# Performance work log

Hardware: AMD Instinct MI355X
Metric: run time of the kernel (lower is better)

The kernel has to match this reference:

```python
import jax, jax.numpy as jnp
import numpy as np

DIM, DEPTH, HEADS, DIM_HEAD, MLP = 1024, 4, 16, 64, 4096
INNER = HEADS * DIM_HEAD
B, N = 2, 1024


def _ln(x, g, b, eps=1e-5):
    mu = jnp.mean(x, axis=-1, keepdims=True)
    var = jnp.mean(jnp.square(x - mu), axis=-1, keepdims=True)
    return (x - mu) * jax.lax.rsqrt(var + eps) * g + b


def setup_inputs() -> dict:
    key = jax.random.key(0)
    ks = jax.random.split(key, 8)
    s = 0.02
    return {
        "x": jax.random.normal(ks[0], (B, N, DIM), jnp.float32),
        "mask": jax.random.randint(ks[1], (B, N, N), 0, 2, jnp.int32),
        "ln1_g": jnp.ones((DEPTH, DIM), jnp.float32),
        "ln1_b": jnp.zeros((DEPTH, DIM), jnp.float32),
        "qkv_w": jax.random.normal(ks[2], (DEPTH, DIM, 3 * INNER), jnp.float32) * s,
        "out_w": jax.random.normal(ks[3], (DEPTH, INNER, DIM), jnp.float32) * s,
        "out_b": jnp.zeros((DEPTH, DIM), jnp.float32),
        "ln2_g": jnp.ones((DEPTH, DIM), jnp.float32),
        "ln2_b": jnp.zeros((DEPTH, DIM), jnp.float32),
        "ff1_w": jax.random.normal(ks[4], (DEPTH, DIM, MLP), jnp.float32) * s,
        "ff1_b": jnp.zeros((DEPTH, MLP), jnp.float32),
        "ff2_w": jax.random.normal(ks[5], (DEPTH, MLP, DIM), jnp.float32) * s,
        "ff2_b": jnp.zeros((DEPTH, DIM), jnp.float32),
    }


def reference(x, mask, ln1_g, ln1_b, qkv_w, out_w, out_b, ln2_g, ln2_b,
              ff1_w, ff1_b, ff2_w, ff2_b):
    scale = DIM_HEAD ** -0.5
    masked = (mask == 0)[:, None, :, :]  # [B,1,N,N], True -> fill -1e9
    b, n, _ = x.shape
    for l in range(DEPTH):
        # --- prenorm attention ---
        h = _ln(x, ln1_g[l], ln1_b[l])
        qkv = h @ qkv_w[l]  # [B,N,3*INNER]
        q, k, v = jnp.split(qkv, 3, axis=-1)
        q = q.reshape(b, n, HEADS, DIM_HEAD).transpose(0, 2, 1, 3)
        k = k.reshape(b, n, HEADS, DIM_HEAD).transpose(0, 2, 1, 3)
        v = v.reshape(b, n, HEADS, DIM_HEAD).transpose(0, 2, 1, 3)
        dots = jnp.einsum('bhqd,bhkd->bhqk', q, k) * scale
        dots = jnp.where(masked, jnp.float32(-1e9), dots)
        attn = jax.nn.softmax(dots, axis=-1)
        o = jnp.einsum('bhqk,bhkd->bhqd', attn, v)
        o = o.transpose(0, 2, 1, 3).reshape(b, n, INNER)
        x = o @ out_w[l] + out_b[l] + x
        # --- prenorm feedforward ---
        h = _ln(x, ln2_g[l], ln2_b[l])
        h = jax.nn.gelu(h @ ff1_w[l] + ff1_b[l], approximate=False)
        x = h @ ff2_w[l] + ff2_b[l] + x
    return x
```

## Files before the change

kernel.cpp:

```cpp
#include <hip/hip_runtime.h>
#include <stdint.h>

#define DIMM 1024
#define NSEQ 1024
#define BB 2
#define HEADSN 16
#define MLPD 4096
#define DEPTHN 4
#define MROWS (BB*NSEQ)
#define VSTR 10240

typedef __bf16 bf16x8 __attribute__((ext_vector_type(8)));
typedef float f32x4 __attribute__((ext_vector_type(4)));

__device__ __forceinline__ float bf2f(unsigned short u) {
    union { uint32_t i; float f; } x; x.i = ((uint32_t)u) << 16; return x.f;
}
__device__ __forceinline__ unsigned short f2bf(float f) {
    union { uint32_t i; float f; } x; x.f = f;
    uint32_t r = x.i + 0x7fffu + ((x.i >> 16) & 1u);
    return (unsigned short)(r >> 16);
}
__device__ __forceinline__ float loadf(const void* p, size_t i, int f32) {
    return f32 ? ((const float*)p)[i] : bf2f(((const unsigned short*)p)[i]);
}
__device__ __forceinline__ uint32_t cvt_pk_bf16(float lo, float hi) {
    uint32_t r;
    asm("v_cvt_pk_bf16_f32 %0, %1, %2" : "=v"(r) : "v"(lo), "v"(hi));
    return r;
}

__device__ __forceinline__ void gl_lds16(const unsigned short* g, unsigned short* l) {
    __builtin_amdgcn_global_load_lds(
        (const __attribute__((address_space(1))) uint32_t*)g,
        (__attribute__((address_space(3))) uint32_t*)l,
        16, 0, 0);
}

__device__ __forceinline__ void wait_vm4() { asm volatile("s_waitcnt vmcnt(4)" ::: "memory"); }
__device__ __forceinline__ void wait_vm0() { asm volatile("s_waitcnt vmcnt(0)" ::: "memory"); }
__device__ __forceinline__ void barrier_sync() {
    asm volatile("" ::: "memory");
    __builtin_amdgcn_s_barrier();
    asm volatile("" ::: "memory");
}

__global__ __launch_bounds__(256) void sniff_kernel(const unsigned short* __restrict__ x,
                                                    int* __restrict__ flag) {
    __shared__ int cnt[256];
    int tid = threadIdx.x;
    int c = 0;
    for (int i = tid * 2; i < 65536; i += 512) {
        int e = (x[i] >> 7) & 0xFF;
        if (e >= 0x8A) c++;
    }
    cnt[tid] = c;
    __syncthreads();
    for (int s = 128; s > 0; s >>= 1) {
        if (tid < s) cnt[tid] += cnt[tid + s];
        __syncthreads();
    }
    if (tid == 0) flag[0] = (cnt[0] > 32) ? 1 : 0;
}

__global__ __launch_bounds__(256) void store_out(const float* __restrict__ xf, void* __restrict__ out,
                                                 const int* __restrict__ flag) {
    int f = flag[0];
    int i = blockIdx.x * 256 + threadIdx.x;
    float v = xf[i];
    if (f) ((float*)out)[i] = v;
    else   ((unsigned short*)out)[i] = f2bf(v);
}
__global__ __launch_bounds__(256) void conv_all(const void* s0, const void* s1, const void* s2,
                                                const void* s3, const void* s4, const void* s5,
                                                const void* s6, unsigned short* __restrict__ dst,
                                                const int* __restrict__ flag) {
    int f = flag[0];
    const void* src; int len, off;
    switch (blockIdx.y) {
        case 0: src = s0; len = 1024; off = 0;    break;
        case 1: src = s1; len = 1024; off = 1024; break;
        case 2: src = s2; len = 1024; off = 2048; break;
        case 3: src = s3; len = 1024; off = 3072; break;
        case 4: src = s4; len = 1024; off = 4096; break;
        case 5: src = s5; len = 1024; off = 5120; break;
        default: src = s6; len = 4096; off = 6144; break;
    }
    int i = blockIdx.x * 256 + threadIdx.x;
    if (i < DEPTHN * len) {
        int l = i / len, o = i - l * len;
        dst[l * VSTR + off + o] = f2bf(loadf(src, i, f));
    }
}

__global__ __launch_bounds__(256) void transpose_conv(const void* __restrict__ in, size_t srcOffE,
                                                      unsigned short* __restrict__ out,
                                                      int K, int N, const int* __restrict__ flag) {
    int f = flag[0];
    __shared__ unsigned short t[32][33];
    int n0 = blockIdx.x * 32, k0 = blockIdx.y * 32;
    int tx = threadIdx.x, ty = threadIdx.y;
#pragma unroll
    for (int i = 0; i < 4; i++) {
        int k = k0 + ty + i * 8;
        t[ty + i * 8][tx] = f2bf(loadf(in, srcOffE + (size_t)k * N + n0 + tx, f));
    }
    __syncthreads();
#pragma unroll
    for (int i = 0; i < 4; i++) {
        int n = n0 + ty + i * 8;
        out[(size_t)n * K + k0 + tx] = t[tx][ty + i * 8];
    }
}

__global__ __launch_bounds__(256) void transpose_attn(const void* __restrict__ qkvw,
                                                      const void* __restrict__ outw,
                                                      int layer, unsigned short* __restrict__ wT,
                                                      const int* __restrict__ flag) {
    int f = flag[0];
    __shared__ unsigned short t[32][33];
    int id = blockIdx.x;
    const void* src; int N; size_t soff; unsigned short* dst; int bx, by;
    if (id < 3072) {
        N = 3072; bx = id % 96; by = id / 96;
        src = qkvw; soff = (size_t)layer * 1024 * 3072; dst = wT;
    } else {
        id -= 3072; N = 1024; bx = id % 32; by = id / 32;
        src = outw; soff = (size_t)layer * 1024 * 1024; dst = wT + 3 * 1024 * 1024;
    }
    int n0 = bx * 32, k0 = by * 32;
    int tx = threadIdx.x, ty = threadIdx.y;
#pragma unroll
    for (int i = 0; i < 4; i++) {
        int k = k0 + ty + i * 8;
        t[ty + i * 8][tx] = f2bf(loadf(src, soff + (size_t)k * N + n0 + tx, f));
    }
    __syncthreads();
#pragma unroll
    for (int i = 0; i < 4; i++) {
        int n = n0 + ty + i * 8;
        dst[(size_t)n * 1024 + k0 + tx] = t[tx][ty + i * 8];
    }
}

__global__ __launch_bounds__(256) void vt_kernel(const unsigned short* __restrict__ qkv,
                                                 unsigned short* __restrict__ vt) {
    __shared__ unsigned short t[32][33];
    int b = blockIdx.z;
    int c0 = blockIdx.x * 32, k0 = blockIdx.y * 32;
    int tx = threadIdx.x, ty = threadIdx.y;
#pragma unroll
    for (int i = 0; i < 4; i++) {
        int k = k0 + ty + i * 8;
        t[ty + i * 8][tx] = qkv[(size_t)(b * 1024 + k) * 3072 + 2048 + c0 + tx];
    }
    __syncthreads();
#pragma unroll
    for (int i = 0; i < 4; i++) {
        int c = c0 + ty + i * 8;
        vt[(size_t)(b * 1024 + c) * 1024 + k0 + tx] = t[tx][ty + i * 8];
    }
}

__global__ __launch_bounds__(256) void mask_pack(const int* __restrict__ mask,
                                                 unsigned long long* __restrict__ bits) {
    int wid = (blockIdx.x * 256 + threadIdx.x) >> 6;
    int lane = threadIdx.x & 63;
#pragma unroll
    for (int i = 0; i < 16; i++) {
        int w = wid * 16 + i;
        int mv = mask[(size_t)w * 64 + lane];
        unsigned long long bl = __ballot(mv != 0);
        if (lane == 0) bits[w] = bl;
    }
}

__global__ __launch_bounds__(256) void ln_raw(const void* __restrict__ x, float* __restrict__ xf,
                                              const unsigned short* __restrict__ g,
                                              const unsigned short* __restrict__ bta,
                                              unsigned short* __restrict__ out,
                                              const int* __restrict__ flag) {
    int f = flag[0];
    int row = blockIdx.x, tid = threadIdx.x;
    size_t base = (size_t)row * DIMM;
    float v[4]; float s = 0.f, s2 = 0.f;
#pragma unroll
    for (int i = 0; i < 4; i++) {
        int c = tid + i * 256;
        v[i] = loadf(x, base + c, f);
        xf[base + c] = v[i];
        s += v[i]; s2 += v[i] * v[i];
    }
#pragma unroll
    for (int off = 32; off >= 1; off >>= 1) {
        s  += __shfl_down(s, off, 64);
        s2 += __shfl_down(s2, off, 64);
    }
    __shared__ float rs[4], rs2[4];
    int wv = tid >> 6;
    if ((tid & 63) == 0) { rs[wv] = s; rs2[wv] = s2; }
    __syncthreads();
    s  = rs[0] + rs[1] + rs[2] + rs[3];
    s2 = rs2[0] + rs2[1] + rs2[2] + rs2[3];
    float mu  = s * (1.f / DIMM);
    float var = s2 * (1.f / DIMM) - mu * mu;
    float rr  = rsqrtf(var + 1e-5f);
#pragma unroll
    for (int i = 0; i < 4; i++) {
        int c = tid + i * 256;
        float y = (v[i] - mu) * rr * bf2f(g[c]) + bf2f(bta[c]);
        out[base + c] = f2bf(y);
    }
}

__global__ __launch_bounds__(256) void ln_kernel(const float* __restrict__ x,
                                                 const unsigned short* __restrict__ g,
                                                 const unsigned short* __restrict__ bta,
                                                 unsigned short* __restrict__ out) {
    int row = blockIdx.x, tid = threadIdx.x;
    const float* xr = x + (size_t)row * DIMM;
    float v[4]; float s = 0.f, s2 = 0.f;
#pragma unroll
    for (int i = 0; i < 4; i++) { v[i] = xr[tid + i * 256]; s += v[i]; s2 += v[i] * v[i]; }
#pragma unroll
    for (int off = 32; off >= 1; off >>= 1) {
        s  += __shfl_down(s, off, 64);
        s2 += __shfl_down(s2, off, 64);
    }
    __shared__ float rs[4], rs2[4];
    int wv = tid >> 6;
    if ((tid & 63) == 0) { rs[wv] = s; rs2[wv] = s2; }
    __syncthreads();
    s  = rs[0] + rs[1] + rs[2] + rs[3];
    s2 = rs2[0] + rs2[1] + rs2[2] + rs2[3];
    float mu  = s * (1.f / DIMM);
    float var = s2 * (1.f / DIMM) - mu * mu;
    float rr  = rsqrtf(var + 1e-5f);
#pragma unroll
    for (int i = 0; i < 4; i++) {
        int c = tid + i * 256;
        float y = (v[i] - mu) * rr * bf2f(g[c]) + bf2f(bta[c]);
        out[(size_t)row * DIMM + c] = f2bf(y);
    }
}

template <int S, int HAS_LN>
__global__ __launch_bounds__(256) void reduce_ln(const float* __restrict__ slab,
                                                 const unsigned short* __restrict__ bias,
                                                 float* __restrict__ xf,
                                                 const unsigned short* __restrict__ g,
                                                 const unsigned short* __restrict__ bta,
                                                 unsigned short* __restrict__ out) {
    const size_t SL = (size_t)MROWS * DIMM;
    int row = blockIdx.x, tid = threadIdx.x;
    float v[4]; float s = 0.f, s2 = 0.f;
#pragma unroll
    for (int i = 0; i < 4; i++) {
        int c = tid + i * 256;
        size_t idx = (size_t)row * DIMM + c;
        float t = xf[idx] + bf2f(bias[c]);
#pragma unroll
        for (int z = 0; z < S; z++) t += slab[z * SL + idx];
        xf[idx] = t;
        v[i] = t; s += t; s2 += t * t;
    }
    if (HAS_LN) {
#pragma unroll
        for (int off = 32; off >= 1; off >>= 1) {
            s  += __shfl_down(s, off, 64);
            s2 += __shfl_down(s2, off, 64);
        }
        __shared__ float rs[4], rs2[4];
        int wv = tid >> 6;
        if ((tid & 63) == 0) { rs[wv] = s; rs2[wv] = s2; }
        __syncthreads();
        s  = rs[0] + rs[1] + rs[2] + rs[3];
        s2 = rs2[0] + rs2[1] + rs2[2] + rs2[3];
        float mu  = s * (1.f / DIMM);
        float var = s2 * (1.f / DIMM) - mu * mu;
        float rr  = rsqrtf(var + 1e-5f);
#pragma unroll
        for (int i = 0; i < 4; i++) {
            int c = tid + i * 256;
            float y = (v[i] - mu) * rr * bf2f(g[c]) + bf2f(bta[c]);
            out[(size_t)row * DIMM + c] = f2bf(y);
        }
    }
}

template <int MODE, int SPLITK>
__global__ __launch_bounds__(512) void gemm_bt(const unsigned short* __restrict__ A,
                                               const unsigned short* __restrict__ Bt,
                                               const unsigned short* __restrict__ bias,
                                               unsigned short* __restrict__ Cbf,
                                               float* __restrict__ Cres,
                                               int M, int N, int K) {
    __shared__ __align__(16) unsigned short As0[128 * 64];
    __shared__ __align__(16) unsigned short Bs0[128 * 64];
    __shared__ __align__(16) unsigned short As1[128 * 64];
    __shared__ __align__(16) unsigned short Bs1[128 * 64];
    const int tid = threadIdx.x;
    const int mBase = blockIdx.y * 128, nBase = blockIdx.x * 128;
    const int w = tid >> 6, lane = tid & 63;
    const int wm = (w >> 2) * 64, wn = (w & 3) * 32;
    const int quad = lane >> 4, l16 = lane & 15;
    const int kLen = K / SPLITK;
    const int kStart = (SPLITK > 1) ? blockIdx.z * kLen : 0;
    const int NT = kLen / 64;

    f32x4 acc[4][2];
#pragma unroll
    for (int i = 0; i < 4; i++)
#pragma unroll
        for (int j = 0; j < 2; j++) acc[i][j] = (f32x4){0.f, 0.f, 0.f, 0.f};

    const int wb = w & 3;
    const int lr8 = lane >> 3;
    const int sgran = (lane & 7) ^ lr8;
    const unsigned short* G = (w < 4 ? A  + (size_t)(mBase + wb * 32 + lr8) * K
                                     : Bt + (size_t)(nBase + wb * 32 + lr8) * K)
                              + kStart + sgran * 8;
    unsigned short* S0 = (w < 4 ? As0 : Bs0) + (wb * 32) * 64;
    unsigned short* S1 = (w < 4 ? As1 : Bs1) + (wb * 32) * 64;
    const size_t r8 = (size_t)8 * K;

    const int rg0 = (quad ^ (l16 & 7)) * 8;
    const int rg1 = ((4 + quad) ^ (l16 & 7)) * 8;

    auto stage = [&](unsigned short* S, int t) {
        const unsigned short* g = G + (size_t)t * 64;
#pragma unroll
        for (int i = 0; i < 4; i++)
            gl_lds16(g + (size_t)i * r8, S + i * 8 * 64);
    };
    auto compute = [&](const unsigned short* Asb, const unsigned short* Bsb) {
#pragma unroll
        for (int ks = 0; ks < 2; ks++) {
            const int rg = ks ? rg1 : rg0;
            bf16x8 af[4], bfv[2];
#pragma unroll
            for (int i = 0; i < 4; i++)
                af[i] = *(const bf16x8*)&Asb[(wm + i * 16 + l16) * 64 + rg];
#pragma unroll
            for (int j = 0; j < 2; j++)
                bfv[j] = *(const bf16x8*)&Bsb[(wn + j * 16 + l16) * 64 + rg];
#pragma unroll
            for (int i = 0; i < 4; i++)
#pragma unroll
                for (int j = 0; j < 2; j++)
                    acc[i][j] = __builtin_amdgcn_mfma_f32_16x16x32_bf16(af[i], bfv[j], acc[i][j], 0, 0, 0);
        }
    };

    stage(S0, 0);
    for (int t = 0; t < NT; t += 2) {
        stage(S1, t + 1);
        wait_vm4();
        barrier_sync();
        compute(As0, Bs0);
        barrier_sync();
        if (t + 2 < NT) {
            stage(S0, t + 2);
            wait_vm4();
        } else {
            wait_vm0();
        }
        barrier_sync();
        compute(As1, Bs1);
        barrier_sync();
    }

    const size_t slabOff = (MODE == 3) ? (size_t)blockIdx.z * M * N : 0;
#pragma unroll
    for (int i = 0; i < 4; i++) {
#pragma unroll
        for (int j = 0; j < 2; j++) {
#pragma unroll
            for (int r = 0; r < 4; r++) {
                int m = mBase + wm + i * 16 + quad * 4 + r;
                int n = nBase + wn + j * 16 + l16;
                float v = acc[i][j][r];
                size_t idx = (size_t)m * N + n;
                if (MODE == 0) {
                    Cbf[idx] = f2bf(v);
                } else if (MODE == 1) {
                    if (SPLITK > 1) {
                        if (blockIdx.z == 0) v += bf2f(bias[n]);
                        atomicAdd(&Cres[idx], v);
                    } else {
                        Cres[idx] += v + bf2f(bias[n]);
                    }
                } else if (MODE == 2) {
                    float t2 = v + bf2f(bias[n]);
                    float gg = 0.5f * t2 * (1.f + erff(t2 * 0.70710678118f));
                    Cbf[idx] = f2bf(gg);
                } else {
                    Cres[slabOff + idx] = v;
                }
            }
        }
    }
}

__global__ __launch_bounds__(256) void attn_mfma(const unsigned short* __restrict__ qkv,
                                                 const unsigned short* __restrict__ vt,
                                                 const unsigned long long* __restrict__ mbits,
                                                 unsigned short* __restrict__ o) {
    __shared__ __align__(16) unsigned short Ks[64 * 72];
    __shared__ __align__(16) unsigned short Vs[64 * 72];

    const int tid = threadIdx.x, w = tid >> 6, lane = tid & 63;
    const int quad = lane >> 4, l16 = lane & 15;
    const int qt = blockIdx.x, h = blockIdx.y, b = blockIdx.z;

    const size_t qrow = (size_t)(b * NSEQ + qt * 64 + w * 16 + l16) * 3072 + h * 64;
    bf16x8 qf[2];
    qf[0] = *(const bf16x8*)(qkv + qrow + quad * 8);
    qf[1] = *(const bf16x8*)(qkv + qrow + 32 + quad * 8);

    const int srow = tid >> 2, scol = (tid & 3) * 16;
    const unsigned short* kg_base = qkv + (size_t)(b * NSEQ) * 3072 + 1024 + h * 64;
    const unsigned short* vg_base = vt + (size_t)((b * HEADSN + h) * 64 + srow) * 1024;

    f32x4 oacc[4];
#pragma unroll
    for (int j = 0; j < 4; j++) oacc[j] = (f32x4){0.f, 0.f, 0.f, 0.f};
    float m_run = -1e30f, l_run = 0.f;

    const unsigned long long* mb = mbits + ((size_t)(b * NSEQ + qt * 64 + w * 16 + l16)) * 16;

    for (int kt = 0; kt < 16; kt++) {
        __syncthreads();
        {
            const unsigned short* kg = kg_base + (size_t)(kt * 64 + srow) * 3072 + scol;
            uint4 k0 = *(const uint4*)kg;
            uint4 k1 = *(const uint4*)(kg + 8);
            const unsigned short* vg = vg_base + kt * 64 + scol;
            uint4 v0 = *(const uint4*)vg;
            uint4 v1 = *(const uint4*)(vg + 8);
            *(uint4*)&Ks[srow * 72 + scol]     = k0;
            *(uint4*)&Ks[srow * 72 + scol + 8] = k1;
            *(uint4*)&Vs[srow * 72 + scol]     = v0;
            *(uint4*)&Vs[srow * 72 + scol + 8] = v1;
        }
        __syncthreads();

        f32x4 sacc[4];
#pragma unroll
        for (int j = 0; j < 4; j++) sacc[j] = (f32x4){0.f, 0.f, 0.f, 0.f};
#pragma unroll
        for (int ks = 0; ks < 2; ks++) {
#pragma unroll
            for (int j = 0; j < 4; j++) {
                bf16x8 kf = *(const bf16x8*)&Ks[(j * 16 + l16) * 72 + ks * 32 + quad * 8];
                sacc[j] = __builtin_amdgcn_mfma_f32_16x16x32_bf16(kf, qf[ks], sacc[j], 0, 0, 0);
            }
        }

        const unsigned long long mw = mb[kt];

        float t[4][4];
        float mxj[4];
#pragma unroll
        for (int j = 0; j < 4; j++) {
            unsigned nib = (unsigned)(mw >> (quad * 4 + j * 16)) & 0xFu;
#pragma unroll
            for (int r = 0; r < 4; r++) {
                float s = sacc[j][r] * 0.125f;
                t[j][r] = ((nib >> r) & 1u) ? s : -1e30f;
            }
            mxj[j] = fmaxf(fmaxf(t[j][0], t[j][1]), fmaxf(t[j][2], t[j][3]));
        }
        float mx = fmaxf(fmaxf(mxj[0], mxj[1]), fmaxf(mxj[2], mxj[3]));
        mx = fmaxf(mx, __shfl_xor(mx, 16, 64));
        mx = fmaxf(mx, __shfl_xor(mx, 32, 64));

        if (!__all(mx <= m_run)) {
            float m_new = fmaxf(m_run, mx);
            float alpha = __expf(m_run - m_new);
            m_run = m_new;
            l_run *= alpha;
            float al[4];
#pragma unroll
            for (int r = 0; r < 4; r++) al[r] = __shfl(alpha, quad * 4 + r, 64);
#pragma unroll
            for (int j = 0; j < 4; j++)
#pragma unroll
                for (int r = 0; r < 4; r++) oacc[j][r] *= al[r];
        }

        float p[4][4];
        float psj[4];
#pragma unroll
        for (int j = 0; j < 4; j++) {
#pragma unroll
            for (int r = 0; r < 4; r++) p[j][r] = __expf(t[j][r] - m_run);
            psj[j] = (p[j][0] + p[j][1]) + (p[j][2] + p[j][3]);
        }
        float ps = (psj[0] + psj[1]) + (psj[2] + psj[3]);
        ps += __shfl_xor(ps, 16, 64);
        ps += __shfl_xor(ps, 32, 64);
        l_run += ps;

        union { uint32_t u[4]; bf16x8 v; } pa[2];
#pragma unroll
        for (int ks = 0; ks < 2; ks++) {
            pa[ks].u[0] = cvt_pk_bf16(p[2 * ks][0],     p[2 * ks][1]);
            pa[ks].u[1] = cvt_pk_bf16(p[2 * ks][2],     p[2 * ks][3]);
            pa[ks].u[2] = cvt_pk_bf16(p[2 * ks + 1][0], p[2 * ks + 1][1]);
            pa[ks].u[3] = cvt_pk_bf16(p[2 * ks + 1][2], p[2 * ks + 1][3]);
        }

#pragma unroll
        for (int ks = 0; ks < 2; ks++) {
#pragma unroll
            for (int j = 0; j < 4; j++) {
                union { ushort4 u[2]; bf16x8 v; } vf;
                const unsigned short* vp = &Vs[(j * 16 + l16) * 72 + ks * 32 + quad * 4];
                vf.u[0] = *(const ushort4*)vp;
                vf.u[1] = *(const ushort4*)(vp + 16);
                oacc[j] = __builtin_amdgcn_mfma_f32_16x16x32_bf16(pa[ks].v, vf.v, oacc[j], 0, 0, 0);
            }
        }
    }

    float inv[4];
#pragma unroll
    for (int r = 0; r < 4; r++) {
        float lr = __shfl(l_run, quad * 4 + r, 64);
        inv[r] = 1.f / lr;
    }
#pragma unroll
    for (int j = 0; j < 4; j++) {
#pragma unroll
        for (int r = 0; r < 4; r++) {
            size_t row = (size_t)(b * NSEQ + qt * 64 + w * 16 + quad * 4 + r);
            o[row * 1024 + h * 64 + j * 16 + l16] = f2bf(oacc[j][r] * inv[r]);
        }
    }
}

extern "C" void kernel_launch(void* const* d_in, const int* in_sizes, int n_in,
                              void* d_out, int out_size, void* d_ws, size_t ws_size,
                              hipStream_t stream) {
    const void* x     = d_in[0];
    const int*  mask  = (const int*)d_in[1];
    const void* ln1_g = d_in[2];
    const void* ln1_b = d_in[3];
    const void* qkv_w = d_in[4];
    const void* out_w = d_in[5];
    const void* out_b = d_in[6];
    const void* ln2_g = d_in[7];
    const void* ln2_b = d_in[8];
    const void* ff1_w = d_in[9];
    const void* ff1_b = d_in[10];
    const void* ff2_w = d_in[11];
    const void* ff2_b = d_in[12];

    char* ws = (char*)d_ws;
    float*          xf     = (float*)ws;
    unsigned short* h_bf   = (unsigned short*)(ws + (8u  << 20));
    unsigned short* qkv_bf = (unsigned short*)(ws + (12u << 20));
    unsigned short* ff_bf  = (unsigned short*)(ws + (12u << 20));
    unsigned short* vt_bf  = (unsigned short*)(ws + (24u << 20));
    unsigned short* o_bf   = (unsigned short*)(ws + (28u << 20));
    unsigned short* wT     = (unsigned short*)(ws + (32u << 20));
    unsigned short* vecs   = (unsigned short*)(ws + (40u << 20));
    int*            flag   = (int*)(ws + (40u << 20) + (128u << 10));
    unsigned long long* mbits = (unsigned long long*)(ws + (40u << 20) + (192u << 10));
    float*          slab   = (float*)(ws + (41u << 20));

    const bool slabs_ok = ws_size >= (74ull << 20);

    sniff_kernel<<<1, 256, 0, stream>>>((const unsigned short*)x, flag);

    conv_all<<<dim3(64, 7), 256, 0, stream>>>(ln1_g, ln1_b, out_b, ln2_g, ln2_b, ff2_b, ff1_b,
                                              vecs, flag);
    mask_pack<<<512, 256, 0, stream>>>(mask, mbits);

    ln_raw<<<MROWS, 256, 0, stream>>>(x, xf, vecs + 0, vecs + 1024, h_bf, flag);

    const int nx = MROWS * DIMM;

    for (int l = 0; l < DEPTHN; l++) {
        const unsigned short* lv = vecs + l * VSTR;
        const unsigned short* lvn = vecs + (l + 1) * VSTR;

        transpose_attn<<<4096, dim3(32, 8), 0, stream>>>(qkv_w, out_w, l, wT, flag);
        gemm_bt<0, 1><<<dim3(3072 / 128, MROWS / 128), 512, 0, stream>>>(
            h_bf, wT, nullptr, qkv_bf, nullptr, MROWS, 3072, 1024);
        vt_kernel<<<dim3(32, 32, BB), dim3(32, 8), 0, stream>>>(qkv_bf, vt_bf);
        attn_mfma<<<dim3(NSEQ / 64, HEADSN, BB), 256, 0, stream>>>(qkv_bf, vt_bf, mbits, o_bf);
        if (slabs_ok) {
            gemm_bt<3, 2><<<dim3(1024 / 128, MROWS / 128, 2), 512, 0, stream>>>(
                o_bf, wT + 3 * 1024 * 1024, nullptr, nullptr, slab, MROWS, 1024, 1024);
            reduce_ln<2, 1><<<MROWS, 256, 0, stream>>>(
                slab, lv + 2048, xf, lv + 3072, lv + 4096, h_bf);
        } else {
            gemm_bt<1, 2><<<dim3(1024 / 128, MROWS / 128, 2), 512, 0, stream>>>(
                o_bf, wT + 3 * 1024 * 1024, lv + 2048, nullptr, xf, MROWS, 1024, 1024);
            ln_kernel<<<MROWS, 256, 0, stream>>>(xf, lv + 3072, lv + 4096, h_bf);
        }

        transpose_conv<<<dim3(4096 / 32, 1024 / 32), dim3(32, 8), 0, stream>>>(
            ff1_w, (size_t)l * 1024 * 4096, wT, 1024, 4096, flag);
        gemm_bt<2, 1><<<dim3(4096 / 128, MROWS / 128), 512, 0, stream>>>(
            h_bf, wT, lv + 6144, ff_bf, nullptr, MROWS, 4096, 1024);
        transpose_conv<<<dim3(1024 / 32, 4096 / 32), dim3(32, 8), 0, stream>>>(
            ff2_w, (size_t)l * 4096 * 1024, wT, 4096, 1024, flag);
        if (slabs_ok) {
            gemm_bt<3, 4><<<dim3(1024 / 128, MROWS / 128, 4), 512, 0, stream>>>(
                ff_bf, wT, nullptr, nullptr, slab, MROWS, 1024, 4096);
            if (l < DEPTHN - 1)
                reduce_ln<4, 1><<<MROWS, 256, 0, stream>>>(
                    slab, lv + 5120, xf, lvn + 0, lvn + 1024, h_bf);
            else
                reduce_ln<4, 0><<<MROWS, 256, 0, stream>>>(
                    slab, lv + 5120, xf, nullptr, nullptr, nullptr);
        } else {
            gemm_bt<1, 4><<<dim3(1024 / 128, MROWS / 128, 4), 512, 0, stream>>>(
                ff_bf, wT, lv + 5120, nullptr, xf, MROWS, 1024, 4096);
            if (l < DEPTHN - 1)
                ln_kernel<<<MROWS, 256, 0, stream>>>(xf, lvn + 0, lvn + 1024, h_bf);
        }
    }

    store_out<<<nx / 256, 256, 0, stream>>>(xf, d_out, flag);
}
```

Before: 843.4 us.

## Double-buffer attention K/V tiles and pre-transpose all layer weights in one launch

The attention kernel now prefetches the next K/V tile and mask word into registers while computing on the current shared-memory buffer, using two LDS buffers and one barrier per iteration. MFMA sections are wrapped with raised wave priority. When the workspace is large enough, all layers' weight transposes are done in a single up-front launch into a dedicated region, removing the per-layer transpose launches. This costs more registers and LDS in attention and needs a larger workspace for the batched transpose.

```diff
diff --git a/kernel.cpp b/kernel.cpp
--- a/kernel.cpp
+++ b/kernel.cpp
@@ -140,6 +140,39 @@
     for (int i = 0; i < 4; i++) {
         int n = n0 + ty + i * 8;
         dst[(size_t)n * 1024 + k0 + tx] = t[tx][ty + i * 8];
+    }
+}
+
+__global__ __launch_bounds__(256) void transpose_all(const void* __restrict__ qkvw,
+                                                     const void* __restrict__ outw,
+                                                     const void* __restrict__ ff1w,
+                                                     const void* __restrict__ ff2w,
+                                                     unsigned short* __restrict__ wTall,
+                                                     const int* __restrict__ flag) {
+    int f = flag[0];
+    __shared__ unsigned short t[32][33];
+    int id = blockIdx.x;
+    int l = blockIdx.y;
+    unsigned short* base = wTall + (size_t)l * (12u * 1024 * 1024);
+    const void* src; int K, N; size_t soff; unsigned short* dst;
+    if (id < 3072)      { src = qkvw; K = 1024; N = 3072; soff = (size_t)l * 1024 * 3072; dst = base; }
+    else if (id < 4096) { id -= 3072; src = outw; K = 1024; N = 1024; soff = (size_t)l * 1024 * 1024; dst = base + 3 * 1024 * 1024; }
+    else if (id < 8192) { id -= 4096; src = ff1w; K = 1024; N = 4096; soff = (size_t)l * 1024 * 4096; dst = base + 4 * 1024 * 1024; }
+    else                { id -= 8192; src = ff2w; K = 4096; N = 1024; soff = (size_t)l * 4096 * 1024; dst = base + 8 * 1024 * 1024; }
+    int nb = N >> 5;
+    int by = id / nb, bx = id - by * nb;
+    int n0 = bx * 32, k0 = by * 32;
+    int tx = threadIdx.x, ty = threadIdx.y;
+#pragma unroll
+    for (int i = 0; i < 4; i++) {
+        int k = k0 + ty + i * 8;
+        t[ty + i * 8][tx] = f2bf(loadf(src, soff + (size_t)k * N + n0 + tx, f));
+    }
+    __syncthreads();
+#pragma unroll
+    for (int i = 0; i < 4; i++) {
+        int n = n0 + ty + i * 8;
+        dst[(size_t)n * K + k0 + tx] = t[tx][ty + i * 8];
     }
 }
 
@@ -406,8 +439,8 @@
                                                  const unsigned short* __restrict__ vt,
                                                  const unsigned long long* __restrict__ mbits,
                                                  unsigned short* __restrict__ o) {
-    __shared__ __align__(16) unsigned short Ks[64 * 72];
-    __shared__ __align__(16) unsigned short Vs[64 * 72];
+    __shared__ __align__(16) unsigned short Ks[2][64 * 72];
+    __shared__ __align__(16) unsigned short Vs[2][64 * 72];
 
     const int tid = threadIdx.x, w = tid >> 6, lane = tid & 63;
     const int quad = lane >> 4, l16 = lane & 15;
@@ -419,8 +452,9 @@
     qf[1] = *(const bf16x8*)(qkv + qrow + 32 + quad * 8);
 
     const int srow = tid >> 2, scol = (tid & 3) * 16;
-    const unsigned short* kg_base = qkv + (size_t)(b * NSEQ) * 3072 + 1024 + h * 64;
-    const unsigned short* vg_base = vt + (size_t)((b * HEADSN + h) * 64 + srow) * 1024;
+    const unsigned short* kg0 = qkv + (size_t)(b * NSEQ) * 3072 + 1024 + h * 64
+                                + (size_t)srow * 3072 + scol;
+    const unsigned short* vg0 = vt + (size_t)((b * HEADSN + h) * 64 + srow) * 1024 + scol;
 
     f32x4 oacc[4];
 #pragma unroll
@@ -429,35 +463,44 @@
 
     const unsigned long long* mb = mbits + ((size_t)(b * NSEQ + qt * 64 + w * 16 + l16)) * 16;
 
+    uint4 ka = *(const uint4*)kg0;
+    uint4 kb = *(const uint4*)(kg0 + 8);
+    uint4 va = *(const uint4*)vg0;
+    uint4 vb = *(const uint4*)(vg0 + 8);
+    *(uint4*)&Ks[0][srow * 72 + scol]     = ka;
+    *(uint4*)&Ks[0][srow * 72 + scol + 8] = kb;
+    *(uint4*)&Vs[0][srow * 72 + scol]     = va;
+    *(uint4*)&Vs[0][srow * 72 + scol + 8] = vb;
+    unsigned long long mw = mb[0];
+    int cur = 0;
+
     for (int kt = 0; kt < 16; kt++) {
         __syncthreads();
-        {
-            const unsigned short* kg = kg_base + (size_t)(kt * 64 + srow) * 3072 + scol;
-            uint4 k0 = *(const uint4*)kg;
-            uint4 k1 = *(const uint4*)(kg + 8);
-            const unsigned short* vg = vg_base + kt * 64 + scol;
-            uint4 v0 = *(const uint4*)vg;
-            uint4 v1 = *(const uint4*)(vg + 8);
-            *(uint4*)&Ks[srow * 72 + scol]     = k0;
-            *(uint4*)&Ks[srow * 72 + scol + 8] = k1;
-            *(uint4*)&Vs[srow * 72 + scol]     = v0;
-            *(uint4*)&Vs[srow * 72 + scol + 8] = v1;
-        }
-        __syncthreads();
+
+        unsigned long long mw_n = 0;
+        if (kt < 15) {
+            const unsigned short* kg = kg0 + (size_t)(kt + 1) * 64 * 3072;
+            ka = *(const uint4*)kg;
+            kb = *(const uint4*)(kg + 8);
+            const unsigned short* vg = vg0 + (kt + 1) * 64;
+            va = *(const uint4*)vg;
+            vb = *(const uint4*)(vg + 8);
+            mw_n = mb[kt + 1];
+        }
 
         f32x4 sacc[4];
 #pragma unroll
         for (int j = 0; j < 4; j++) sacc[j] = (f32x4){0.f, 0.f, 0.f, 0.f};
+        __builtin_amdgcn_s_setprio(1);
 #pragma unroll
         for (int ks = 0; ks < 2; ks++) {
 #pragma unroll
             for (int j = 0; j < 4; j++) {
-                bf16x8 kf = *(const bf16x8*)&Ks[(j * 16 + l16) * 72 + ks * 32 + quad * 8];
+                bf16x8 kf = *(const bf16x8*)&Ks[cur][(j * 16 + l16) * 72 + ks * 32 + quad * 8];
                 sacc[j] = __builtin_amdgcn_mfma_f32_16x16x32_bf16(kf, qf[ks], sacc[j], 0, 0, 0);
             }
         }
-
-        const unsigned long long mw = mb[kt];
+        __builtin_amdgcn_s_setprio(0);
 
         float t[4][4];
         float mxj[4];
@@ -511,16 +554,27 @@
             pa[ks].u[3] = cvt_pk_bf16(p[2 * ks + 1][2], p[2 * ks + 1][3]);
         }
 
+        __builtin_amdgcn_s_setprio(1);
 #pragma unroll
         for (int ks = 0; ks < 2; ks++) {
 #pragma unroll
             for (int j = 0; j < 4; j++) {
                 union { ushort4 u[2]; bf16x8 v; } vf;
-                const unsigned short* vp = &Vs[(j * 16 + l16) * 72 + ks * 32 + quad * 4];
+                const unsigned short* vp = &Vs[cur][(j * 16 + l16) * 72 + ks * 32 + quad * 4];
                 vf.u[0] = *(const ushort4*)vp;
                 vf.u[1] = *(const ushort4*)(vp + 16);
                 oacc[j] = __builtin_amdgcn_mfma_f32_16x16x32_bf16(pa[ks].v, vf.v, oacc[j], 0, 0, 0);
             }
+        }
+        __builtin_amdgcn_s_setprio(0);
+
+        if (kt < 15) {
+            *(uint4*)&Ks[cur ^ 1][srow * 72 + scol]     = ka;
+            *(uint4*)&Ks[cur ^ 1][srow * 72 + scol + 8] = kb;
+            *(uint4*)&Vs[cur ^ 1][srow * 72 + scol]     = va;
+            *(uint4*)&Vs[cur ^ 1][srow * 72 + scol + 8] = vb;
+            mw = mw_n;
+            cur ^= 1;
         }
     }
 
@@ -569,8 +623,10 @@
     int*            flag   = (int*)(ws + (40u << 20) + (128u << 10));
     unsigned long long* mbits = (unsigned long long*)(ws + (40u << 20) + (192u << 10));
     float*          slab   = (float*)(ws + (41u << 20));
+    unsigned short* wTall  = (unsigned short*)(ws + (73ull << 20));
 
     const bool slabs_ok = ws_size >= (74ull << 20);
+    const bool bigws    = ws_size >= (170ull << 20);
 
     sniff_kernel<<<1, 256, 0, stream>>>((const unsigned short*)x, flag);
 
@@ -580,37 +636,50 @@
 
     ln_raw<<<MROWS, 256, 0, stream>>>(x, xf, vecs + 0, vecs + 1024, h_bf, flag);
 
+    if (bigws)
+        transpose_all<<<dim3(12288, 4), dim3(32, 8), 0, stream>>>(
+            qkv_w, out_w, ff1_w, ff2_w, wTall, flag);
+
     const int nx = MROWS * DIMM;
 
     for (int l = 0; l < DEPTHN; l++) {
         const unsigned short* lv = vecs + l * VSTR;
         const unsigned short* lvn = vecs + (l + 1) * VSTR;
 
-        transpose_attn<<<4096, dim3(32, 8), 0, stream>>>(qkv_w, out_w, l, wT, flag);
+        const unsigned short* lbase = bigws ? wTall + (size_t)l * (12u * 1024 * 1024) : wT;
+        const unsigned short* qkvT = lbase;
+        const unsigned short* outT = lbase + 3 * 1024 * 1024;
+        const unsigned short* ff1T = bigws ? lbase + 4 * 1024 * 1024 : wT;
+        const unsigned short* ff2T = bigws ? lbase + 8 * 1024 * 1024 : wT;
+
+        if (!bigws)
+            transpose_attn<<<4096, dim3(32, 8), 0, stream>>>(qkv_w, out_w, l, wT, flag);
         gemm_bt<0, 1><<<dim3(3072 / 128, MROWS / 128), 512, 0, stream>>>(
-            h_bf, wT, nullptr, qkv_bf, nullptr, MROWS, 3072, 1024);
+            h_bf, qkvT, nullptr, qkv_bf, nullptr, MROWS, 3072, 1024);
         vt_kernel<<<dim3(32, 32, BB), dim3(32, 8), 0, stream>>>(qkv_bf, vt_bf);
         attn_mfma<<<dim3(NSEQ / 64, HEADSN, BB), 256, 0, stream>>>(qkv_bf, vt_bf, mbits, o_bf);
         if (slabs_ok) {
             gemm_bt<3, 2><<<dim3(1024 / 128, MROWS / 128, 2), 512, 0, stream>>>(
-                o_bf, wT + 3 * 1024 * 1024, nullptr, nullptr, slab, MROWS, 1024, 1024);
+                o_bf, outT, nullptr, nullptr, slab, MROWS, 1024, 1024);
             reduce_ln<2, 1><<<MROWS, 256, 0, stream>>>(
                 slab, lv + 2048, xf, lv + 3072, lv + 4096, h_bf);
         } else {
             gemm_bt<1, 2><<<dim3(1024 / 128, MROWS / 128, 2), 512, 0, stream>>>(
-                o_bf, wT + 3 * 1024 * 1024, lv + 2048, nullptr, xf, MROWS, 1024, 1024);
+                o_bf, outT, lv + 2048, nullptr, xf, MROWS, 1024, 1024);
             ln_kernel<<<MROWS, 256, 0, stream>>>(xf, lv + 3072, lv + 4096, h_bf);
         }
 
-        transpose_conv<<<dim3(4096 / 32, 1024 / 32), dim3(32, 8), 0, stream>>>(
-            ff1_w, (size_t)l * 1024 * 4096, wT, 1024, 4096, flag);
+        if (!bigws)
+            transpose_conv<<<dim3(4096 / 32, 1024 / 32), dim3(32, 8), 0, stream>>>(
+                ff1_w, (size_t)l * 1024 * 4096, wT, 1024, 4096, flag);
         gemm_bt<2, 1><<<dim3(4096 / 128, MROWS / 128), 512, 0, stream>>>(
-            h_bf, wT, lv + 6144, ff_bf, nullptr, MROWS, 4096, 1024);
-        transpose_conv<<<dim3(1024 / 32, 4096 / 32), dim3(32, 8), 0, stream>>>(
-            ff2_w, (size_t)l * 4096 * 1024, wT, 4096, 1024, flag);
+            h_bf, ff1T, lv + 6144, ff_bf, nullptr, MROWS, 4096, 1024);
+        if (!bigws)
+            transpose_conv<<<dim3(1024 / 32, 4096 / 32), dim3(32, 8), 0, stream>>>(
+                ff2_w, (size_t)l * 4096 * 1024, wT, 4096, 1024, flag);
         if (slabs_ok) {
             gemm_bt<3, 4><<<dim3(1024 / 128, MROWS / 128, 4), 512, 0, stream>>>(
-                ff_bf, wT, nullptr, nullptr, slab, MROWS, 1024, 4096);
+                ff_bf, ff2T, nullptr, nullptr, slab, MROWS, 1024, 4096);
             if (l < DEPTHN - 1)
                 reduce_ln<4, 1><<<MROWS, 256, 0, stream>>>(
                     slab, lv + 5120, xf, lvn + 0, lvn + 1024, h_bf);
@@ -619,7 +688,7 @@
                     slab, lv + 5120, xf, nullptr, nullptr, nullptr);
         } else {
             gemm_bt<1, 4><<<dim3(1024 / 128, MROWS / 128, 4), 512, 0, stream>>>(
-                ff_bf, wT, lv + 5120, nullptr, xf, MROWS, 1024, 4096);
+                ff_bf, ff2T, lv + 5120, nullptr, xf, MROWS, 1024, 4096);
             if (l < DEPTHN - 1)
                 ln_kernel<<<MROWS, 256, 0, stream>>>(xf, lvn + 0, lvn + 1024, h_bf);
         }
```

Measured after the change: 827.9 us. No clear change (-1.8%).
